# Optimization experiments

Measured on AMD Instinct MI355X. Metric: run time of the kernel, lower is better.

Reference implementation:

```python
import jax, jax.numpy as jnp
import numpy as np


def _local_conv2d(x, w, b):
    """Untied (locally connected) conv, stride 1, VALID.
    x: (B, C, H, W); w: (1, O, C, Ho, Wo, k*k); b: (1, O, Ho, Wo) or None.
    Matches torch: x.unfold(2,k).unfold(3,k) -> (B,C,Ho,Wo,k,k) flattened (k*k),
    then (x[:,None] * w).sum([2,-1]) + b.
    """
    B, C, H, W = x.shape
    Ho, Wo = w.shape[3], w.shape[4]
    kh = H - Ho + 1
    kw = W - Wo + 1
    # patches: (B, C*kh*kw, Ho, Wo), feature dim ordered (C, kh, kw) — same as torch unfold
    patches = jax.lax.conv_general_dilated_patches(x, (kh, kw), (1, 1), 'VALID')
    patches = patches.reshape(B, C, kh * kw, Ho, Wo)
    out = jnp.einsum('bckhw,ochwk->bohw', patches, w[0])
    if b is not None:
        out = out + b
    return out


def _maxpool2(x):
    return jax.lax.reduce_window(x, -jnp.inf, jax.lax.max,
                                 (1, 1, 2, 2), (1, 1, 2, 2), 'VALID')


def setup_inputs() -> dict:
    key = jax.random.key(0)
    ks = jax.random.split(key, 11)
    B, C, H, W = 1024, 3, 32, 32
    s = lambda k, shape, fan: jax.random.normal(k, shape, jnp.float32) * np.sqrt(2.0 / fan)
    return {
        'x': jax.random.normal(ks[0], (B, C, H, W), jnp.float32),
        'w1': s(ks[1], (1, 6, 3, 28, 28, 25), 3 * 25),
        'b1': s(ks[2], (1, 6, 28, 28), 28 * 28) ,
        'w2': s(ks[3], (1, 16, 6, 10, 10, 25), 6 * 25),
        'b2': s(ks[4], (1, 16, 10, 10), 10 * 10),
        'w3': s(ks[5], (1, 120, 16, 1, 1, 25), 16 * 25),
        'b3': s(ks[6], (1, 120, 1, 1), 1),
        'fc2_w': s(ks[7], (84, 120), 120),
        'fc2_b': jnp.zeros((84,), jnp.float32),
        'fc3_w': s(ks[8], (10, 84), 84),
        'fc3_b': jnp.zeros((10,), jnp.float32),
    }


def reference(x, w1, b1, w2, b2, w3, b3, fc2_w, fc2_b, fc3_w, fc3_b):
    h = _maxpool2(jax.nn.relu(_local_conv2d(x, w1, b1)))   # (B,6,14,14)
    h = _maxpool2(jax.nn.relu(_local_conv2d(h, w2, b2)))   # (B,16,5,5)
    h = jax.nn.relu(_local_conv2d(h, w3, b3))              # (B,120,1,1)
    h = h.reshape(h.shape[0], -1)                          # (B,120)
    h = jax.nn.relu(h @ fc2_w.T + fc2_b)                   # (B,84)
    return h @ fc3_w.T + fc3_b                             # (B,10)
```

## Files before the change

### kernel.cpp

```cpp
#include <hip/hip_runtime.h>
#include <math.h>

#define NB 1024

__global__ __launch_bounds__(256) void k_transpose(const float* __restrict__ x,
                                                   float* __restrict__ xT) {
  __shared__ float tile[64][65];
  const int c0 = blockIdx.x * 64;
  const int b0 = blockIdx.y * 64;
  const int tx = threadIdx.x & 63;
  const int ty = threadIdx.x >> 6;
#pragma unroll
  for (int r = 0; r < 16; ++r) {
    const int bb = r * 4 + ty;
    tile[bb][tx] = x[(size_t)(b0 + bb) * 3072 + c0 + tx];
  }
  __syncthreads();
#pragma unroll
  for (int r = 0; r < 16; ++r) {
    const int cc = r * 4 + ty;
    xT[(size_t)(c0 + cc) * NB + b0 + tx] = tile[tx][cc];
  }
}

__global__ __launch_bounds__(256) void k_conv1(const float* __restrict__ xT,
                                               const float* __restrict__ w1,
                                               const float* __restrict__ b1,
                                               float* __restrict__ h1) {
  const int w = blockIdx.x;
  const int xcd = w & 7, k = w >> 3;
  const int bg = xcd >> 1;
  const int pos = (xcd & 1) * 98 + k;
  const int ph = pos / 14, pw = pos % 14;
  const int b = bg * 256 + threadIdx.x;

  __shared__ __align__(16) float wL[72 * 28];
  __shared__ float bL[24];
  for (int t = threadIdx.x; t < 72 * 25; t += 256) {
    const int chunk = t / 25, p = t - chunk * 25;
    const int o = chunk / 12, rem = chunk - o * 12;
    const int c = rem >> 2, i = (rem >> 1) & 1, j = rem & 1;
    wL[chunk * 28 + p] =
        w1[((size_t)((o * 3 + c) * 28 + (2 * ph + i)) * 28 + (2 * pw + j)) * 25 + p];
  }
  if (threadIdx.x < 24) {
    const int o = threadIdx.x >> 2, i = (threadIdx.x >> 1) & 1, j = threadIdx.x & 1;
    bL[threadIdx.x] = b1[(size_t)(o * 28 + (2 * ph + i)) * 28 + (2 * pw + j)];
  }
  __syncthreads();

  float acc[6][2][2];
#pragma unroll
  for (int o = 0; o < 6; ++o)
#pragma unroll
    for (int i = 0; i < 2; ++i)
#pragma unroll
      for (int j = 0; j < 2; ++j) acc[o][i][j] = 0.f;

  for (int c = 0; c < 3; ++c) {
    float xw[6][6];
#pragma unroll
    for (int dh = 0; dh < 6; ++dh)
#pragma unroll
      for (int dw = 0; dw < 6; ++dw)
        xw[dh][dw] =
            xT[((size_t)(c * 32 + (2 * ph + dh)) * 32 + (2 * pw + dw)) * NB + b];
#pragma unroll
    for (int o = 0; o < 6; ++o)
#pragma unroll
      for (int i = 0; i < 2; ++i)
#pragma unroll
        for (int j = 0; j < 2; ++j) {
          const float* wp = &wL[((o * 3 + c) * 4 + i * 2 + j) * 28];
#pragma unroll
          for (int p = 0; p < 25; ++p)
            acc[o][i][j] = fmaf(xw[i + p / 5][j + p % 5], wp[p], acc[o][i][j]);
        }
  }

#pragma unroll
  for (int o = 0; o < 6; ++o) {
    float v[2][2];
#pragma unroll
    for (int i = 0; i < 2; ++i)
#pragma unroll
      for (int j = 0; j < 2; ++j)
        v[i][j] = fmaxf(acc[o][i][j] + bL[o * 4 + i * 2 + j], 0.f);
    const float m = fmaxf(fmaxf(v[0][0], v[0][1]), fmaxf(v[1][0], v[1][1]));
    h1[((size_t)(o * 14 + ph) * 14 + pw) * NB + b] = m;
  }
}

__global__ __launch_bounds__(256) void k_conv2(const float* __restrict__ h1,
                                               const float* __restrict__ w2,
                                               const float* __restrict__ b2,
                                               float* __restrict__ h2) {
  const int w = blockIdx.x;
  const int xcd = w & 7, k = w >> 3;
  const int bg = xcd >> 1;
  const int unit = (xcd & 1) * 100 + k;
  const int og = unit / 25;
  const int pos = unit % 25;
  const int ph = pos / 5, pw = pos % 5;
  const int b = bg * 256 + threadIdx.x;

  __shared__ __align__(16) float wL[48 * 28];
  __shared__ float bL[8];
  for (int t = threadIdx.x; t < 48 * 25; t += 256) {
    const int chunk = t / 25, p = t - chunk * 25;
    const int oo = chunk / 24, rem = chunk - oo * 24;
    const int c = rem >> 2, i = (rem >> 1) & 1, j = rem & 1;
    const int o = og * 2 + oo;
    wL[chunk * 28 + p] =
        w2[((size_t)((o * 6 + c) * 10 + (2 * ph + i)) * 10 + (2 * pw + j)) * 25 + p];
  }
  if (threadIdx.x < 8) {
    const int oo = threadIdx.x >> 2, i = (threadIdx.x >> 1) & 1, j = threadIdx.x & 1;
    const int o = og * 2 + oo;
    bL[threadIdx.x] = b2[(size_t)(o * 10 + (2 * ph + i)) * 10 + (2 * pw + j)];
  }
  __syncthreads();

  float acc[2][2][2];
#pragma unroll
  for (int oo = 0; oo < 2; ++oo)
#pragma unroll
    for (int i = 0; i < 2; ++i)
#pragma unroll
      for (int j = 0; j < 2; ++j) acc[oo][i][j] = 0.f;

  for (int c = 0; c < 6; ++c) {
    float xw[6][6];
#pragma unroll
    for (int dh = 0; dh < 6; ++dh)
#pragma unroll
      for (int dw = 0; dw < 6; ++dw)
        xw[dh][dw] =
            h1[((size_t)(c * 14 + (2 * ph + dh)) * 14 + (2 * pw + dw)) * NB + b];
#pragma unroll
    for (int oo = 0; oo < 2; ++oo)
#pragma unroll
      for (int i = 0; i < 2; ++i)
#pragma unroll
        for (int j = 0; j < 2; ++j) {
          const float* wp = &wL[((oo * 6 + c) * 4 + i * 2 + j) * 28];
#pragma unroll
          for (int p = 0; p < 25; ++p)
            acc[oo][i][j] = fmaf(xw[i + p / 5][j + p % 5], wp[p], acc[oo][i][j]);
        }
  }

#pragma unroll
  for (int oo = 0; oo < 2; ++oo) {
    const int o = og * 2 + oo;
    float v[2][2];
#pragma unroll
    for (int i = 0; i < 2; ++i)
#pragma unroll
      for (int j = 0; j < 2; ++j)
        v[i][j] = fmaxf(acc[oo][i][j] + bL[oo * 4 + i * 2 + j], 0.f);
    const float m = fmaxf(fmaxf(v[0][0], v[0][1]), fmaxf(v[1][0], v[1][1]));
    h2[((size_t)(o * 5 + ph) * 5 + pw) * NB + b] = m;
  }
}

__global__ __launch_bounds__(256) void k_conv3(const float* __restrict__ h2,
                                               const float* __restrict__ w3,
                                               const float* __restrict__ b3,
                                               float* __restrict__ h3) {
  const int w = blockIdx.x;
  const int xcd = w & 7, k2 = w >> 3;
  const int bg = xcd >> 1;
  const int o = (xcd & 1) * 60 + k2;
  const int b = bg * 256 + threadIdx.x;
  __shared__ __align__(16) float wL[400];
  for (int t = threadIdx.x; t < 400; t += 256) wL[t] = w3[(size_t)o * 400 + t];
  __syncthreads();

  float a0 = 0.f, a1 = 0.f, a2 = 0.f, a3 = 0.f;
#pragma unroll 8
  for (int k = 0; k < 400; k += 4) {
    a0 = fmaf(h2[(size_t)(k + 0) * NB + b], wL[k + 0], a0);
    a1 = fmaf(h2[(size_t)(k + 1) * NB + b], wL[k + 1], a1);
    a2 = fmaf(h2[(size_t)(k + 2) * NB + b], wL[k + 2], a2);
    a3 = fmaf(h2[(size_t)(k + 3) * NB + b], wL[k + 3], a3);
  }
  h3[(size_t)o * NB + b] = fmaxf((a0 + a1) + (a2 + a3) + b3[o], 0.f);
}

__global__ __launch_bounds__(256) void k_fctail(const float* __restrict__ h3,
                                                const float* __restrict__ fc2w,
                                                const float* __restrict__ fc2b,
                                                const float* __restrict__ fc3w,
                                                const float* __restrict__ fc3b,
                                                float* __restrict__ out) {
  const int b0 = blockIdx.x * 16;
  const int tid = threadIdx.x;
  __shared__ float h3L[120 * 16];
  __shared__ float h4L[84 * 16];

  for (int t = tid; t < 120 * 16; t += 256) {
    const int k = t >> 4, bb = t & 15;
    h3L[t] = h3[(size_t)k * NB + b0 + bb];
  }
  __syncthreads();

  const int bb = tid & 15;
  {
    const int jbase = tid >> 4;
#pragma unroll
    for (int jr = 0; jr < 6; ++jr) {
      const int j = jbase + jr * 16;
      if (j < 84) {
        const float* __restrict__ wp = fc2w + (size_t)j * 120;
        float a0 = 0.f, a1 = 0.f;
#pragma unroll
        for (int k = 0; k < 120; k += 2) {
          a0 = fmaf(h3L[(k + 0) * 16 + bb], wp[k + 0], a0);
          a1 = fmaf(h3L[(k + 1) * 16 + bb], wp[k + 1], a1);
        }
        h4L[j * 16 + bb] = fmaxf(a0 + a1 + fc2b[j], 0.f);
      }
    }
  }
  __syncthreads();

  if (tid < 160) {
    const int i = tid >> 4;
    const float* __restrict__ wp = fc3w + (size_t)i * 84;
    float a0 = 0.f, a1 = 0.f;
#pragma unroll
    for (int j = 0; j < 84; j += 2) {
      a0 = fmaf(h4L[(j + 0) * 16 + bb], wp[j + 0], a0);
      a1 = fmaf(h4L[(j + 1) * 16 + bb], wp[j + 1], a1);
    }
    out[(size_t)(b0 + bb) * 10 + i] = a0 + a1 + fc3b[i];
  }
}

extern "C" void kernel_launch(void* const* d_in, const int* in_sizes, int n_in,
                              void* d_out, int out_size, void* d_ws, size_t ws_size,
                              hipStream_t stream) {
  const float* x    = (const float*)d_in[0];
  const float* w1   = (const float*)d_in[1];
  const float* b1   = (const float*)d_in[2];
  const float* w2   = (const float*)d_in[3];
  const float* b2   = (const float*)d_in[4];
  const float* w3   = (const float*)d_in[5];
  const float* b3   = (const float*)d_in[6];
  const float* fc2w = (const float*)d_in[7];
  const float* fc2b = (const float*)d_in[8];
  const float* fc3w = (const float*)d_in[9];
  const float* fc3b = (const float*)d_in[10];
  float* out = (float*)d_out;

  float* ws = (float*)d_ws;
  float* xT = ws;
  float* h1 = xT + 3145728;
  float* h2 = h1 + 1204224;
  float* h3 = h2 + 409600;

  k_transpose<<<dim3(48, 16), 256, 0, stream>>>(x, xT);
  k_conv1<<<dim3(784), 256, 0, stream>>>(xT, w1, b1, h1);
  k_conv2<<<dim3(800), 256, 0, stream>>>(h1, w2, b2, h2);
  k_conv3<<<dim3(480), 256, 0, stream>>>(h2, w3, b3, h3);
  k_fctail<<<dim3(64), 256, 0, stream>>>(h3, fc2w, fc2b, fc3w, fc3b, out);
}
```

Before: 168.3 us.

## Split conv work across pool quadrants and K segments with float2 batch pairs

In conv1 and conv2, each wavefront now computes one of the four 2x2 pooling positions, and each thread handles two batch elements loaded as float2. Max-pooling is finished through a shared-memory reduction. conv3 splits its 400-long reduction across four wavefronts and computes two output channels per block, with the partial sums combined in shared memory. This doubles the block counts for conv1 and conv2 and cuts per-thread register pressure, aiming for more parallelism and wider memory accesses. The cost is extra syncs, a shared-memory round trip, and redundant loads of the overlapping input windows.

```diff
diff --git a/kernel.cpp b/kernel.cpp
--- a/kernel.cpp
+++ b/kernel.cpp
@@ -27,67 +27,73 @@
                                                const float* __restrict__ w1,
                                                const float* __restrict__ b1,
                                                float* __restrict__ h1) {
-  const int w = blockIdx.x;
-  const int xcd = w & 7, k = w >> 3;
-  const int bg = xcd >> 1;
-  const int pos = (xcd & 1) * 98 + k;
+  const int u = blockIdx.x;
+  const int bg = u & 7;
+  const int pos = u >> 3;
   const int ph = pos / 14, pw = pos % 14;
-  const int b = bg * 256 + threadIdx.x;
+  const int lane = threadIdx.x & 63;
+  const int ij = threadIdx.x >> 6;
+  const int i = ij >> 1, j = ij & 1;
+  const int b = bg * 128 + lane * 2;
 
   __shared__ __align__(16) float wL[72 * 28];
   __shared__ float bL[24];
+  __shared__ float2 pool[4][6][64];
   for (int t = threadIdx.x; t < 72 * 25; t += 256) {
     const int chunk = t / 25, p = t - chunk * 25;
     const int o = chunk / 12, rem = chunk - o * 12;
-    const int c = rem >> 2, i = (rem >> 1) & 1, j = rem & 1;
+    const int c = rem >> 2, ii = (rem >> 1) & 1, jj = rem & 1;
     wL[chunk * 28 + p] =
-        w1[((size_t)((o * 3 + c) * 28 + (2 * ph + i)) * 28 + (2 * pw + j)) * 25 + p];
+        w1[((size_t)((o * 3 + c) * 28 + (2 * ph + ii)) * 28 + (2 * pw + jj)) * 25 + p];
   }
   if (threadIdx.x < 24) {
-    const int o = threadIdx.x >> 2, i = (threadIdx.x >> 1) & 1, j = threadIdx.x & 1;
-    bL[threadIdx.x] = b1[(size_t)(o * 28 + (2 * ph + i)) * 28 + (2 * pw + j)];
-  }
-  __syncthreads();
-
-  float acc[6][2][2];
-#pragma unroll
-  for (int o = 0; o < 6; ++o)
-#pragma unroll
-    for (int i = 0; i < 2; ++i)
-#pragma unroll
-      for (int j = 0; j < 2; ++j) acc[o][i][j] = 0.f;
+    const int o = threadIdx.x >> 2, ii = (threadIdx.x >> 1) & 1, jj = threadIdx.x & 1;
+    bL[threadIdx.x] = b1[(size_t)(o * 28 + (2 * ph + ii)) * 28 + (2 * pw + jj)];
+  }
+  __syncthreads();
+
+  float2 acc[6];
+#pragma unroll
+  for (int o = 0; o < 6; ++o) { acc[o].x = 0.f; acc[o].y = 0.f; }
 
   for (int c = 0; c < 3; ++c) {
-    float xw[6][6];
-#pragma unroll
-    for (int dh = 0; dh < 6; ++dh)
-#pragma unroll
-      for (int dw = 0; dw < 6; ++dw)
-        xw[dh][dw] =
-            xT[((size_t)(c * 32 + (2 * ph + dh)) * 32 + (2 * pw + dw)) * NB + b];
-#pragma unroll
-    for (int o = 0; o < 6; ++o)
-#pragma unroll
-      for (int i = 0; i < 2; ++i)
-#pragma unroll
-        for (int j = 0; j < 2; ++j) {
-          const float* wp = &wL[((o * 3 + c) * 4 + i * 2 + j) * 28];
-#pragma unroll
-          for (int p = 0; p < 25; ++p)
-            acc[o][i][j] = fmaf(xw[i + p / 5][j + p % 5], wp[p], acc[o][i][j]);
-        }
+    float2 xw[25];
+#pragma unroll
+    for (int dh = 0; dh < 5; ++dh)
+#pragma unroll
+      for (int dw = 0; dw < 5; ++dw)
+        xw[dh * 5 + dw] = *reinterpret_cast<const float2*>(
+            &xT[((size_t)(c * 32 + (2 * ph + i + dh)) * 32 + (2 * pw + j + dw)) * NB + b]);
+#pragma unroll
+    for (int o = 0; o < 6; ++o) {
+      const float* wp = &wL[((o * 3 + c) * 4 + ij) * 28];
+#pragma unroll
+      for (int p = 0; p < 25; ++p) {
+        const float wv = wp[p];
+        acc[o].x = fmaf(xw[p].x, wv, acc[o].x);
+        acc[o].y = fmaf(xw[p].y, wv, acc[o].y);
+      }
+    }
   }
 
 #pragma unroll
   for (int o = 0; o < 6; ++o) {
-    float v[2][2];
-#pragma unroll
-    for (int i = 0; i < 2; ++i)
-#pragma unroll
-      for (int j = 0; j < 2; ++j)
-        v[i][j] = fmaxf(acc[o][i][j] + bL[o * 4 + i * 2 + j], 0.f);
-    const float m = fmaxf(fmaxf(v[0][0], v[0][1]), fmaxf(v[1][0], v[1][1]));
-    h1[((size_t)(o * 14 + ph) * 14 + pw) * NB + b] = m;
+    const float bias = bL[o * 4 + ij];
+    float2 v;
+    v.x = fmaxf(acc[o].x + bias, 0.f);
+    v.y = fmaxf(acc[o].y + bias, 0.f);
+    pool[ij][o][lane] = v;
+  }
+  __syncthreads();
+
+  for (int idx = threadIdx.x; idx < 384; idx += 256) {
+    const int o = idx >> 6, l2 = idx & 63;
+    float2 m = pool[0][o][l2];
+    const float2 m1 = pool[1][o][l2], m2 = pool[2][o][l2], m3 = pool[3][o][l2];
+    m.x = fmaxf(fmaxf(m.x, m1.x), fmaxf(m2.x, m3.x));
+    m.y = fmaxf(fmaxf(m.y, m1.y), fmaxf(m2.y, m3.y));
+    *reinterpret_cast<float2*>(
+        &h1[((size_t)(o * 14 + ph) * 14 + pw) * NB + bg * 128 + l2 * 2]) = m;
   }
 }
 
@@ -95,72 +101,77 @@
                                                const float* __restrict__ w2,
                                                const float* __restrict__ b2,
                                                float* __restrict__ h2) {
-  const int w = blockIdx.x;
-  const int xcd = w & 7, k = w >> 3;
-  const int bg = xcd >> 1;
-  const int unit = (xcd & 1) * 100 + k;
-  const int og = unit / 25;
-  const int pos = unit % 25;
+  const int u = blockIdx.x;
+  const int bg = u & 7;
+  const int k = u >> 3;
+  const int og = k / 25;
+  const int pos = k % 25;
   const int ph = pos / 5, pw = pos % 5;
-  const int b = bg * 256 + threadIdx.x;
+  const int lane = threadIdx.x & 63;
+  const int ij = threadIdx.x >> 6;
+  const int i = ij >> 1, j = ij & 1;
+  const int b = bg * 128 + lane * 2;
 
   __shared__ __align__(16) float wL[48 * 28];
   __shared__ float bL[8];
+  __shared__ float2 pool[4][2][64];
   for (int t = threadIdx.x; t < 48 * 25; t += 256) {
     const int chunk = t / 25, p = t - chunk * 25;
     const int oo = chunk / 24, rem = chunk - oo * 24;
-    const int c = rem >> 2, i = (rem >> 1) & 1, j = rem & 1;
+    const int c = rem >> 2, ii = (rem >> 1) & 1, jj = rem & 1;
     const int o = og * 2 + oo;
     wL[chunk * 28 + p] =
-        w2[((size_t)((o * 6 + c) * 10 + (2 * ph + i)) * 10 + (2 * pw + j)) * 25 + p];
+        w2[((size_t)((o * 6 + c) * 10 + (2 * ph + ii)) * 10 + (2 * pw + jj)) * 25 + p];
   }
   if (threadIdx.x < 8) {
-    const int oo = threadIdx.x >> 2, i = (threadIdx.x >> 1) & 1, j = threadIdx.x & 1;
+    const int oo = threadIdx.x >> 2, ii = (threadIdx.x >> 1) & 1, jj = threadIdx.x & 1;
     const int o = og * 2 + oo;
-    bL[threadIdx.x] = b2[(size_t)(o * 10 + (2 * ph + i)) * 10 + (2 * pw + j)];
-  }
-  __syncthreads();
-
-  float acc[2][2][2];
-#pragma unroll
-  for (int oo = 0; oo < 2; ++oo)
-#pragma unroll
-    for (int i = 0; i < 2; ++i)
-#pragma unroll
-      for (int j = 0; j < 2; ++j) acc[oo][i][j] = 0.f;
+    bL[threadIdx.x] = b2[(size_t)(o * 10 + (2 * ph + ii)) * 10 + (2 * pw + jj)];
+  }
+  __syncthreads();
+
+  float2 acc[2];
+  acc[0].x = acc[0].y = acc[1].x = acc[1].y = 0.f;
 
   for (int c = 0; c < 6; ++c) {
-    float xw[6][6];
-#pragma unroll
-    for (int dh = 0; dh < 6; ++dh)
-#pragma unroll
-      for (int dw = 0; dw < 6; ++dw)
-        xw[dh][dw] =
-            h1[((size_t)(c * 14 + (2 * ph + dh)) * 14 + (2 * pw + dw)) * NB + b];
-#pragma unroll
-    for (int oo = 0; oo < 2; ++oo)
-#pragma unroll
-      for (int i = 0; i < 2; ++i)
-#pragma unroll
-        for (int j = 0; j < 2; ++j) {
-          const float* wp = &wL[((oo * 6 + c) * 4 + i * 2 + j) * 28];
-#pragma unroll
-          for (int p = 0; p < 25; ++p)
-            acc[oo][i][j] = fmaf(xw[i + p / 5][j + p % 5], wp[p], acc[oo][i][j]);
-        }
+    float2 xw[25];
+#pragma unroll
+    for (int dh = 0; dh < 5; ++dh)
+#pragma unroll
+      for (int dw = 0; dw < 5; ++dw)
+        xw[dh * 5 + dw] = *reinterpret_cast<const float2*>(
+            &h1[((size_t)(c * 14 + (2 * ph + i + dh)) * 14 + (2 * pw + j + dw)) * NB + b]);
+#pragma unroll
+    for (int oo = 0; oo < 2; ++oo) {
+      const float* wp = &wL[((oo * 6 + c) * 4 + ij) * 28];
+#pragma unroll
+      for (int p = 0; p < 25; ++p) {
+        const float wv = wp[p];
+        acc[oo].x = fmaf(xw[p].x, wv, acc[oo].x);
+        acc[oo].y = fmaf(xw[p].y, wv, acc[oo].y);
+      }
+    }
   }
 
 #pragma unroll
   for (int oo = 0; oo < 2; ++oo) {
+    const float bias = bL[oo * 4 + ij];
+    float2 v;
+    v.x = fmaxf(acc[oo].x + bias, 0.f);
+    v.y = fmaxf(acc[oo].y + bias, 0.f);
+    pool[ij][oo][lane] = v;
+  }
+  __syncthreads();
+
+  if (threadIdx.x < 128) {
+    const int oo = threadIdx.x >> 6, l2 = threadIdx.x & 63;
     const int o = og * 2 + oo;
-    float v[2][2];
-#pragma unroll
-    for (int i = 0; i < 2; ++i)
-#pragma unroll
-      for (int j = 0; j < 2; ++j)
-        v[i][j] = fmaxf(acc[oo][i][j] + bL[oo * 4 + i * 2 + j], 0.f);
-    const float m = fmaxf(fmaxf(v[0][0], v[0][1]), fmaxf(v[1][0], v[1][1]));
-    h2[((size_t)(o * 5 + ph) * 5 + pw) * NB + b] = m;
+    float2 m = pool[0][oo][l2];
+    const float2 m1 = pool[1][oo][l2], m2 = pool[2][oo][l2], m3 = pool[3][oo][l2];
+    m.x = fmaxf(fmaxf(m.x, m1.x), fmaxf(m2.x, m3.x));
+    m.y = fmaxf(fmaxf(m.y, m1.y), fmaxf(m2.y, m3.y));
+    *reinterpret_cast<float2*>(
+        &h2[((size_t)(o * 5 + ph) * 5 + pw) * NB + bg * 128 + l2 * 2]) = m;
   }
 }
 
@@ -168,24 +179,44 @@
                                                const float* __restrict__ w3,
                                                const float* __restrict__ b3,
                                                float* __restrict__ h3) {
-  const int w = blockIdx.x;
-  const int xcd = w & 7, k2 = w >> 3;
-  const int bg = xcd >> 1;
-  const int o = (xcd & 1) * 60 + k2;
-  const int b = bg * 256 + threadIdx.x;
-  __shared__ __align__(16) float wL[400];
-  for (int t = threadIdx.x; t < 400; t += 256) wL[t] = w3[(size_t)o * 400 + t];
-  __syncthreads();
-
-  float a0 = 0.f, a1 = 0.f, a2 = 0.f, a3 = 0.f;
-#pragma unroll 8
-  for (int k = 0; k < 400; k += 4) {
-    a0 = fmaf(h2[(size_t)(k + 0) * NB + b], wL[k + 0], a0);
-    a1 = fmaf(h2[(size_t)(k + 1) * NB + b], wL[k + 1], a1);
-    a2 = fmaf(h2[(size_t)(k + 2) * NB + b], wL[k + 2], a2);
-    a3 = fmaf(h2[(size_t)(k + 3) * NB + b], wL[k + 3], a3);
-  }
-  h3[(size_t)o * NB + b] = fmaxf((a0 + a1) + (a2 + a3) + b3[o], 0.f);
+  const int u = blockIdx.x;
+  const int bg = u & 7;
+  const int o = (u >> 3) * 2;
+  const int lane = threadIdx.x & 63;
+  const int kseg = threadIdx.x >> 6;
+  const int b = bg * 128 + lane * 2;
+
+  __shared__ __align__(16) float wL[2][400];
+  __shared__ float2 kbuf[4][2][64];
+  for (int t = threadIdx.x; t < 800; t += 256) {
+    const int oo = t / 400, p = t - oo * 400;
+    wL[oo][p] = w3[(size_t)(o + oo) * 400 + p];
+  }
+  __syncthreads();
+
+  float2 a0 = {0.f, 0.f}, a1 = {0.f, 0.f};
+  const int k0 = kseg * 100;
+#pragma unroll 4
+  for (int k = k0; k < k0 + 100; ++k) {
+    const float2 xv = *reinterpret_cast<const float2*>(&h2[(size_t)k * NB + b]);
+    const float w0 = wL[0][k], w1v = wL[1][k];
+    a0.x = fmaf(xv.x, w0, a0.x);  a0.y = fmaf(xv.y, w0, a0.y);
+    a1.x = fmaf(xv.x, w1v, a1.x); a1.y = fmaf(xv.y, w1v, a1.y);
+  }
+  kbuf[kseg][0][lane] = a0;
+  kbuf[kseg][1][lane] = a1;
+  __syncthreads();
+
+  if (threadIdx.x < 128) {
+    const int oo = threadIdx.x >> 6, l2 = threadIdx.x & 63;
+    const float2 s0 = kbuf[0][oo][l2], s1 = kbuf[1][oo][l2];
+    const float2 s2 = kbuf[2][oo][l2], s3 = kbuf[3][oo][l2];
+    const float bias = b3[o + oo];
+    float2 r;
+    r.x = fmaxf((s0.x + s1.x) + (s2.x + s3.x) + bias, 0.f);
+    r.y = fmaxf((s0.y + s1.y) + (s2.y + s3.y) + bias, 0.f);
+    *reinterpret_cast<float2*>(&h3[(size_t)(o + oo) * NB + bg * 128 + l2 * 2]) = r;
+  }
 }
 
 __global__ __launch_bounds__(256) void k_fctail(const float* __restrict__ h3,
@@ -261,8 +292,8 @@
   float* h3 = h2 + 409600;
 
   k_transpose<<<dim3(48, 16), 256, 0, stream>>>(x, xT);
-  k_conv1<<<dim3(784), 256, 0, stream>>>(xT, w1, b1, h1);
-  k_conv2<<<dim3(800), 256, 0, stream>>>(h1, w2, b2, h2);
+  k_conv1<<<dim3(1568), 256, 0, stream>>>(xT, w1, b1, h1);
+  k_conv2<<<dim3(1600), 256, 0, stream>>>(h1, w2, b2, h2);
   k_conv3<<<dim3(480), 256, 0, stream>>>(h2, w3, b3, h3);
   k_fctail<<<dim3(64), 256, 0, stream>>>(h3, fc2w, fc2b, fc3w, fc3b, out);
 }
```

After: 171.4 us. No clear change (+1.9%).
